# Kernel tuning notes

Measured on AMD Instinct MI355X. Metric: run time of the kernel, lower is better.

The kernel has to match this reference:

```python
import jax, jax.numpy as jnp
import numpy as np

B, S, I, H = 64, 1024, 1024, 1024


def setup_inputs() -> dict:
    key = jax.random.key(0)
    ks = jax.random.split(key, 14)
    bound = (1.0 / H) ** 0.5
    u = lambda k, shape: jax.random.uniform(k, shape, jnp.float32, -bound, bound)
    return {
        "inputs": jax.random.normal(ks[0], (B, S, I), jnp.float32),
        "hidden_states": jax.random.normal(ks[1], (1, B, H), jnp.float32),
        "w_ir": u(ks[2], (H, I)), "w_iz": u(ks[3], (H, I)), "w_in": u(ks[4], (H, I)),
        "b_ir": u(ks[5], (H,)), "b_iz": u(ks[6], (H,)), "b_in": u(ks[7], (H,)),
        "w_hr": u(ks[8], (H, H)), "w_hz": u(ks[9], (H, H)), "w_hn": u(ks[10], (H, H)),
        "b_hr": u(ks[11], (H,)), "b_hz": u(ks[12], (H,)), "b_hn": u(ks[13], (H,)),
    }


def reference(inputs, hidden_states, w_ir, w_iz, w_in, b_ir, b_iz, b_in,
              w_hr, w_hz, w_hn, b_hr, b_hz, b_hn):
    # Precompute input projections for all timesteps (batched GEMMs), [B,S,H]
    x_ir = jnp.einsum('bsi,hi->bsh', inputs, w_ir) + b_ir
    x_iz = jnp.einsum('bsi,hi->bsh', inputs, w_iz) + b_iz
    x_in = jnp.einsum('bsi,hi->bsh', inputs, w_in) + b_in

    def step(h, xs):
        xr, xz, xn = xs  # each [B,H]
        r = jax.nn.sigmoid(xr + h @ w_hr.T + b_hr)
        z = jax.nn.sigmoid(xz + h @ w_hz.T + b_hz)
        n = jnp.tanh(xn + r * (h @ w_hn.T + b_hn))
        h_new = (1.0 - z) * n + z * h
        return h_new, h_new

    h0 = hidden_states[0]  # [B,H]
    # scan over time: xs leading axis S
    xs = (jnp.swapaxes(x_ir, 0, 1), jnp.swapaxes(x_iz, 0, 1), jnp.swapaxes(x_in, 0, 1))
    h_final, outs = jax.lax.scan(step, h0, xs)
    outputs = jnp.swapaxes(outs, 0, 1)  # [B,S,H]
    return outputs, h_final[None]
```

## Files before the change

### kernel.cpp

```cpp
#include <hip/hip_runtime.h>
#include <hip/hip_bf16.h>

typedef __attribute__((ext_vector_type(8))) short bf16x8;
typedef __attribute__((ext_vector_type(4))) float f32x4;
typedef unsigned short u16;
typedef unsigned int u32;

static constexpr int B_ = 64, S_ = 1024, I_ = 1024, H_ = 1024;

__device__ __forceinline__ u16 f2b(float f) {
  union { float f; unsigned u; } v; v.f = f;
  unsigned r = v.u + 0x7FFF + ((v.u >> 16) & 1);
  return (u16)(r >> 16);
}
__device__ __forceinline__ float b2f(u16 u) {
  union { unsigned u; float f; } v; v.u = ((unsigned)u) << 16;
  return v.f;
}

__device__ __forceinline__ void st_coh_u16(void* p, unsigned v) {
  asm volatile("global_store_short %0, %1, off sc0 sc1" :: "v"(p), "v"(v) : "memory");
}
__device__ __forceinline__ void st_coh_u32(void* p, unsigned v) {
  asm volatile("global_store_dword %0, %1, off sc0 sc1" :: "v"(p), "v"(v) : "memory");
}
__device__ __forceinline__ unsigned ld_coh_u32_wait(const void* p) {
  unsigned r;
  asm volatile("global_load_dword %0, %1, off sc0 sc1\n\ts_waitcnt vmcnt(0)"
               : "=v"(r) : "v"(p) : "memory");
  return r;
}
__device__ __forceinline__ uint4 ld_coh_b128(const void* p) {
  uint4 r;
  asm volatile("global_load_dwordx4 %0, %1, off sc0 sc1" : "=v"(r) : "v"(p) : "memory");
  return r;
}

__global__ void cvt_f32_bf16(const float* __restrict__ src, u16* __restrict__ dst, int n4) {
  int i = blockIdx.x * blockDim.x + threadIdx.x;
  int stride = gridDim.x * blockDim.x;
  for (; i < n4; i += stride) {
    float4 f = ((const float4*)src)[i];
    ushort4 o;
    o.x = f2b(f.x); o.y = f2b(f.y); o.z = f2b(f.z); o.w = f2b(f.w);
    ((ushort4*)dst)[i] = o;
  }
}

__global__ __launch_bounds__(256) void xproj_gemm(
    const u16* __restrict__ A, const u16* __restrict__ W,
    const float* __restrict__ b_ir, const float* __restrict__ b_iz, const float* __restrict__ b_in,
    u16* __restrict__ X) {
  __shared__ u16 smem[16384];
  u16* As = smem;
  u16* Bs = smem + 8192;
  int bid = blockIdx.x;
  int mt = bid / 24; int rr = bid % 24; int g = rr >> 3; int nt = rr & 7;
  int tid = threadIdx.x, lane = tid & 63, wid = tid >> 6;
  int wr = wid >> 1, wc = wid & 1;
  const u16* A0 = A + (size_t)mt * 128 * 1024;
  const u16* W0 = W + (size_t)g * 1024 * 1024 + (size_t)nt * 128 * 1024;
  f32x4 acc[4][4] = {};
  for (int k0 = 0; k0 < 1024; k0 += 64) {
    __syncthreads();
#pragma unroll
    for (int j = 0; j < 4; ++j) {
      int c = wid * 4 + j;
      int row = c * 8 + (lane >> 3);
      int ke = (lane & 7) * 8;
      __builtin_amdgcn_global_load_lds(
          (const __attribute__((address_space(1))) void*)(A0 + row * 1024 + k0 + ke),
          (__attribute__((address_space(3))) void*)(As + c * 512), 16, 0, 0);
      __builtin_amdgcn_global_load_lds(
          (const __attribute__((address_space(1))) void*)(W0 + row * 1024 + k0 + ke),
          (__attribute__((address_space(3))) void*)(Bs + c * 512), 16, 0, 0);
    }
    asm volatile("s_waitcnt vmcnt(0)" ::: "memory");
    __syncthreads();
#pragma unroll
    for (int kk = 0; kk < 64; kk += 32) {
      bf16x8 a[4], b[4];
      int rbase = lane & 15;
      int koff = kk + ((lane >> 4) << 3);
#pragma unroll
      for (int mi = 0; mi < 4; ++mi)
        a[mi] = *(const bf16x8*)(As + (wr * 64 + mi * 16 + rbase) * 64 + koff);
#pragma unroll
      for (int ni = 0; ni < 4; ++ni)
        b[ni] = *(const bf16x8*)(Bs + (wc * 64 + ni * 16 + rbase) * 64 + koff);
#pragma unroll
      for (int mi = 0; mi < 4; ++mi)
#pragma unroll
        for (int ni = 0; ni < 4; ++ni)
          acc[mi][ni] = __builtin_amdgcn_mfma_f32_16x16x32_bf16(a[mi], b[ni], acc[mi][ni], 0, 0, 0);
    }
  }
  __syncthreads();
  const float* bp = (g == 0) ? b_ir : (g == 1) ? b_iz : b_in;
  float bias[4];
#pragma unroll
  for (int ni = 0; ni < 4; ++ni)
    bias[ni] = bp[nt * 128 + wc * 64 + ni * 16 + (lane & 15)];
#pragma unroll
  for (int mi = 0; mi < 4; ++mi)
#pragma unroll
    for (int ni = 0; ni < 4; ++ni) {
      int ml = wr * 64 + mi * 16 + ((lane >> 4) << 2);
      int nl = wc * 64 + ni * 16 + (lane & 15);
#pragma unroll
      for (int i = 0; i < 4; ++i)
        smem[(ml + i) * 128 + nl] = f2b(acc[mi][ni][i] + bias[ni]);
    }
  __syncthreads();
#pragma unroll
  for (int j = 0; j < 8; ++j) {
    int c = tid + j * 256;
    int rowl = c >> 4;
    int n0 = (c & 15) * 8;
    int m = mt * 128 + rowl;
    int b = m >> 10, s = m & 1023;
    bf16x8 v = *(const bf16x8*)(smem + rowl * 128 + n0);
    *(bf16x8*)(X + ((size_t)((s * 64 + b) * 3 + g)) * 1024 + nt * 128 + n0) = v;
  }
}

__global__ __launch_bounds__(256) void gru_scan(
    const u16* __restrict__ xbuf, const float* __restrict__ h0p,
    const float* __restrict__ w_hr, const float* __restrict__ w_hz, const float* __restrict__ w_hn,
    const float* __restrict__ b_hr, const float* __restrict__ b_hz, const float* __restrict__ b_hn,
    u16* __restrict__ hbf, float* __restrict__ out, u32* __restrict__ flags) {
  extern __shared__ u16 smem[];
  u16* Wl = smem;
  u16* Hl = smem + 49152;
  float* ex = (float*)(smem + 65536);
  int tid = threadIdx.x, lane = tid & 63, wid = tid >> 6;
  int wg = blockIdx.x, mq = wg & 3, cb = wg >> 2;
  u32* gflags = flags + mq * 64;

  for (int idx = tid; idx < 3 * 2048; idx += 256) {
    int g = idx >> 11; int rem = idx & 2047; int row = rem >> 7; int ch = rem & 127;
    const float* wsrc = (g == 0) ? w_hr : (g == 1) ? w_hz : w_hn;
    const float* src = wsrc + (size_t)(cb * 16 + row) * 1024 + ch * 8;
    float4 f0 = *(const float4*)src;
    float4 f1 = *(const float4*)(src + 4);
    bf16x8 v;
    v[0] = (short)f2b(f0.x); v[1] = (short)f2b(f0.y); v[2] = (short)f2b(f0.z); v[3] = (short)f2b(f0.w);
    v[4] = (short)f2b(f1.x); v[5] = (short)f2b(f1.y); v[6] = (short)f2b(f1.z); v[7] = (short)f2b(f1.w);
    int kbyte = (ch * 16) ^ ((row & 7) << 4);
    *(bf16x8*)((char*)(Wl + g * 16384) + row * 2048 + kbyte) = v;
  }

  int b_l = tid >> 4, c_l = tid & 15;
  int bg = mq * 16 + b_l, cg = cb * 16 + c_l;
  float h = h0p[bg * 1024 + cg];
  float bhr = b_hr[cg], bhz = b_hz[cg], bhn = b_hn[cg];
  st_coh_u16(hbf + bg * 1024 + cg, f2b(h));
  __syncthreads();
  if (tid == 0) st_coh_u32(gflags + cb, 1u);

  bf16x8 wfrag[32];
  {
    const char* wbase = (const char*)(Wl + (wid < 3 ? wid : 0) * 16384);
    int row = lane & 15;
    int klane = (lane >> 4) << 4;
    int sw = (row & 7) << 4;
#pragma unroll
    for (int ks = 0; ks < 32; ++ks)
      wfrag[ks] = *(const bf16x8*)(wbase + row * 2048 + (((ks << 6) + klane) ^ sw));
  }

  const size_t outb = (size_t)bg * S_ * H_;
  for (int t = 0; t < S_; ++t) {
    const u16* rdbuf = hbf + (size_t)(t & 1) * 65536;
    u16* wrbuf = hbf + (size_t)((t + 1) & 1) * 65536;

    const u16* xp = xbuf + (size_t)(t * 64 + bg) * 3072 + cg;
    u16 xr_u = xp[0], xz_u = xp[1024], xn_u = xp[2048];

    {
      unsigned tgt = (unsigned)(t + 1);
      const u32* fp = gflags + lane;
      unsigned v = ld_coh_u32_wait(fp);
      while (!__all((int)(v >= tgt))) {
        __builtin_amdgcn_s_sleep(1);
        v = ld_coh_u32_wait(fp);
      }
    }

    uint4 tmp[8];
#pragma unroll
    for (int j = 0; j < 8; ++j) {
      int ch2 = tid + j * 256;
      int row = ch2 >> 7, kc = ch2 & 127;
      tmp[j] = ld_coh_b128(rdbuf + (mq * 16 + row) * 1024 + kc * 8);
    }
    asm volatile("s_waitcnt vmcnt(0)" ::: "memory");
    __builtin_amdgcn_sched_barrier(0);
#pragma unroll
    for (int j = 0; j < 8; ++j) {
      int ch2 = tid + j * 256;
      int row = ch2 >> 7, kc = ch2 & 127;
      int kbyte = (kc * 16) ^ ((row & 7) << 4);
      *(uint4*)((char*)Hl + row * 2048 + kbyte) = tmp[j];
    }
    __syncthreads();

    f32x4 acc0 = {}, acc1 = {}, acc2 = {}, acc3 = {};
    if (wid < 3) {
      const char* hbase = (const char*)Hl;
      int row = lane & 15;
      int klane = (lane >> 4) << 4;
      int sw = (row & 7) << 4;
#pragma unroll
      for (int ks = 0; ks < 32; ks += 4) {
#pragma unroll
        for (int q = 0; q < 4; ++q) {
          int off = row * 2048 + ((((ks + q) << 6) + klane) ^ sw);
          bf16x8 av = *(const bf16x8*)(hbase + off);
          if (q == 0) acc0 = __builtin_amdgcn_mfma_f32_16x16x32_bf16(av, wfrag[ks + q], acc0, 0, 0, 0);
          else if (q == 1) acc1 = __builtin_amdgcn_mfma_f32_16x16x32_bf16(av, wfrag[ks + q], acc1, 0, 0, 0);
          else if (q == 2) acc2 = __builtin_amdgcn_mfma_f32_16x16x32_bf16(av, wfrag[ks + q], acc2, 0, 0, 0);
          else acc3 = __builtin_amdgcn_mfma_f32_16x16x32_bf16(av, wfrag[ks + q], acc3, 0, 0, 0);
        }
      }
      f32x4 acc = (acc0 + acc1) + (acc2 + acc3);
      int col = lane & 15, r0 = (lane >> 4) << 2;
#pragma unroll
      for (int i = 0; i < 4; ++i)
        ex[wid * 256 + (r0 + i) * 16 + col] = acc[i];
    }
    __syncthreads();

    float hr = ex[b_l * 16 + c_l] + bhr;
    float hz = ex[256 + b_l * 16 + c_l] + bhz;
    float hn = ex[512 + b_l * 16 + c_l] + bhn;
    float xr = b2f(xr_u), xz = b2f(xz_u), xn = b2f(xn_u);
    float r = 1.f / (1.f + __expf(-(xr + hr)));
    float z = 1.f / (1.f + __expf(-(xz + hz)));
    float nn = 1.f - 2.f / (__expf(2.f * (xn + r * hn)) + 1.f);
    h = (1.f - z) * nn + z * h;
    st_coh_u16(wrbuf + bg * 1024 + cg, f2b(h));
    __syncthreads();
    if (tid == 0) st_coh_u32(gflags + cb, (unsigned)(t + 2));
    out[outb + (size_t)t * H_ + cg] = h;
  }
  out[(size_t)B_ * S_ * H_ + bg * 1024 + cg] = h;
}

extern "C" void kernel_launch(void* const* d_in, const int* in_sizes, int n_in,
                              void* d_out, int out_size, void* d_ws, size_t ws_size,
                              hipStream_t stream) {
  const float* inputs = (const float*)d_in[0];
  const float* h0p    = (const float*)d_in[1];
  const float* w_ir   = (const float*)d_in[2];
  const float* w_iz   = (const float*)d_in[3];
  const float* w_in   = (const float*)d_in[4];
  const float* b_ir   = (const float*)d_in[5];
  const float* b_iz   = (const float*)d_in[6];
  const float* b_in   = (const float*)d_in[7];
  const float* w_hr   = (const float*)d_in[8];
  const float* w_hz   = (const float*)d_in[9];
  const float* w_hn   = (const float*)d_in[10];
  const float* b_hr   = (const float*)d_in[11];
  const float* b_hz   = (const float*)d_in[12];
  const float* b_hn   = (const float*)d_in[13];
  float* out = (float*)d_out;

  size_t xbytes  = (size_t)S_ * B_ * 3 * H_ * 2;
  size_t wibytes = (size_t)3 * H_ * I_ * 2;
  size_t hbytes  = (size_t)2 * B_ * H_ * 2;
  size_t flagbytes = 1024;
  if (ws_size < xbytes + wibytes + hbytes + flagbytes) return;

  u16* xbuf = (u16*)d_ws;
  u16* wibf = (u16*)((char*)d_ws + xbytes);
  u16* hbf  = (u16*)((char*)d_ws + xbytes + wibytes);
  u32* flags = (u32*)((char*)d_ws + xbytes + wibytes + hbytes);
  u16* Abf  = (u16*)d_out;

  (void)hipMemsetAsync(flags, 0, flagbytes, stream);

  cvt_f32_bf16<<<2048, 256, 0, stream>>>(inputs, Abf, B_ * S_ * I_ / 4);
  cvt_f32_bf16<<<256, 256, 0, stream>>>(w_ir, wibf,               H_ * I_ / 4);
  cvt_f32_bf16<<<256, 256, 0, stream>>>(w_iz, wibf + H_ * I_,     H_ * I_ / 4);
  cvt_f32_bf16<<<256, 256, 0, stream>>>(w_in, wibf + 2 * H_ * I_, H_ * I_ / 4);

  xproj_gemm<<<12288, 256, 0, stream>>>(Abf, wibf, b_ir, b_iz, b_in, xbuf);

  (void)hipFuncSetAttribute((const void*)gru_scan, hipFuncAttributeMaxDynamicSharedMemorySize, 135168);
  gru_scan<<<dim3(256), dim3(256), 134144, stream>>>(
      xbuf, h0p, w_hr, w_hz, w_hn, b_hr, b_hz, b_hn, hbf, out, flags);
}
```

Measured before the change: 4.592 ms.

## Replace per-step flag barrier with timestep-tagged hidden-state words polled directly

Each hidden-state element is now stored as a 32-bit word holding its bf16 value plus the timestep tag in the upper half. Consumers poll the data itself until every tag matches, instead of waiting on a per-block flag that was written after a block-wide syncthreads. This removes the extra syncthreads, the separate flag store, and the flag-then-data round trip on each step. A per-wave consumption flag guards against the double buffer being overwritten too early. In exchange the hidden-state traffic doubles, and the whole 16-row read is retried on every failed poll.

```diff
diff --git a/kernel.cpp b/kernel.cpp
--- a/kernel.cpp
+++ b/kernel.cpp
@@ -18,17 +18,8 @@
   return v.f;
 }
 
-__device__ __forceinline__ void st_coh_u16(void* p, unsigned v) {
-  asm volatile("global_store_short %0, %1, off sc0 sc1" :: "v"(p), "v"(v) : "memory");
-}
 __device__ __forceinline__ void st_coh_u32(void* p, unsigned v) {
   asm volatile("global_store_dword %0, %1, off sc0 sc1" :: "v"(p), "v"(v) : "memory");
-}
-__device__ __forceinline__ unsigned ld_coh_u32_wait(const void* p) {
-  unsigned r;
-  asm volatile("global_load_dword %0, %1, off sc0 sc1\n\ts_waitcnt vmcnt(0)"
-               : "=v"(r) : "v"(p) : "memory");
-  return r;
 }
 __device__ __forceinline__ uint4 ld_coh_b128(const void* p) {
   uint4 r;
@@ -128,14 +119,13 @@
     const u16* __restrict__ xbuf, const float* __restrict__ h0p,
     const float* __restrict__ w_hr, const float* __restrict__ w_hz, const float* __restrict__ w_hn,
     const float* __restrict__ b_hr, const float* __restrict__ b_hz, const float* __restrict__ b_hn,
-    u16* __restrict__ hbf, float* __restrict__ out, u32* __restrict__ flags) {
+    u32* __restrict__ hbuf, float* __restrict__ out, u32* __restrict__ flags) {
   extern __shared__ u16 smem[];
   u16* Wl = smem;
   u16* Hl = smem + 49152;
   float* ex = (float*)(smem + 65536);
   int tid = threadIdx.x, lane = tid & 63, wid = tid >> 6;
   int wg = blockIdx.x, mq = wg & 3, cb = wg >> 2;
-  u32* gflags = flags + mq * 64;
 
   for (int idx = tid; idx < 3 * 2048; idx += 256) {
     int g = idx >> 11; int rem = idx & 2047; int row = rem >> 7; int ch = rem & 127;
@@ -154,9 +144,8 @@
   int bg = mq * 16 + b_l, cg = cb * 16 + c_l;
   float h = h0p[bg * 1024 + cg];
   float bhr = b_hr[cg], bhz = b_hz[cg], bhn = b_hn[cg];
-  st_coh_u16(hbf + bg * 1024 + cg, f2b(h));
+  st_coh_u32(hbuf + bg * 1024 + cg, (unsigned)f2b(h));
   __syncthreads();
-  if (tid == 0) st_coh_u32(gflags + cb, 1u);
 
   bf16x8 wfrag[32];
   {
@@ -169,39 +158,50 @@
       wfrag[ks] = *(const bf16x8*)(wbase + row * 2048 + (((ks << 6) + klane) ^ sw));
   }
 
+  u32* cfl_self = flags + mq * 256 + wid * 64 + cb;
+  const u32* cfl_poll = flags + mq * 256 + wid * 64 + lane;
   const size_t outb = (size_t)bg * S_ * H_;
+
   for (int t = 0; t < S_; ++t) {
-    const u16* rdbuf = hbf + (size_t)(t & 1) * 65536;
-    u16* wrbuf = hbf + (size_t)((t + 1) & 1) * 65536;
+    const u32* rbase = hbuf + (size_t)(t & 1) * 65536 + (size_t)(mq * 16 + wid * 4) * 1024;
+    u32* wrw = hbuf + (size_t)((t + 1) & 1) * 65536 + bg * 1024 + cg;
 
     const u16* xp = xbuf + (size_t)(t * 64 + bg) * 3072 + cg;
     u16 xr_u = xp[0], xz_u = xp[1024], xn_u = xp[2048];
 
-    {
-      unsigned tgt = (unsigned)(t + 1);
-      const u32* fp = gflags + lane;
-      unsigned v = ld_coh_u32_wait(fp);
-      while (!__all((int)(v >= tgt))) {
-        __builtin_amdgcn_s_sleep(1);
-        v = ld_coh_u32_wait(fp);
+    uint4 tmp[16];
+    unsigned et = (unsigned)t;
+    for (;;) {
+#pragma unroll
+      for (int j = 0; j < 16; ++j) {
+        int cid = j * 64 + lane;
+        int rl = cid >> 8, c4 = cid & 255;
+        tmp[j] = ld_coh_b128(rbase + rl * 1024 + c4 * 4);
       }
-    }
-
-    uint4 tmp[8];
-#pragma unroll
-    for (int j = 0; j < 8; ++j) {
-      int ch2 = tid + j * 256;
-      int row = ch2 >> 7, kc = ch2 & 127;
-      tmp[j] = ld_coh_b128(rdbuf + (mq * 16 + row) * 1024 + kc * 8);
-    }
-    asm volatile("s_waitcnt vmcnt(0)" ::: "memory");
-    __builtin_amdgcn_sched_barrier(0);
-#pragma unroll
-    for (int j = 0; j < 8; ++j) {
-      int ch2 = tid + j * 256;
-      int row = ch2 >> 7, kc = ch2 & 127;
-      int kbyte = (kc * 16) ^ ((row & 7) << 4);
-      *(uint4*)((char*)Hl + row * 2048 + kbyte) = tmp[j];
+      unsigned cf;
+      asm volatile("global_load_dword %0, %1, off sc0 sc1" : "=v"(cf) : "v"(cfl_poll) : "memory");
+      asm volatile("s_waitcnt vmcnt(0)" ::: "memory");
+      __builtin_amdgcn_sched_barrier(0);
+      bool ok = (cf >= et);
+#pragma unroll
+      for (int j = 0; j < 16; ++j)
+        ok = ok & ((tmp[j].x >> 16) == et) & ((tmp[j].y >> 16) == et)
+                & ((tmp[j].z >> 16) == et) & ((tmp[j].w >> 16) == et);
+      if (__all((int)ok)) break;
+      __builtin_amdgcn_s_sleep(1);
+    }
+    if (lane == 0) st_coh_u32(cfl_self, (unsigned)(t + 1));
+
+#pragma unroll
+    for (int j = 0; j < 16; ++j) {
+      int cid = j * 64 + lane;
+      int rl = cid >> 8, c4 = cid & 255;
+      int row = wid * 4 + rl;
+      uint2 pk;
+      pk.x = (tmp[j].x & 0xffffu) | (tmp[j].y << 16);
+      pk.y = (tmp[j].z & 0xffffu) | (tmp[j].w << 16);
+      int kbyte = (c4 * 8) ^ ((row & 7) << 4);
+      *(uint2*)((char*)Hl + row * 2048 + kbyte) = pk;
     }
     __syncthreads();
 
@@ -239,9 +239,7 @@
     float z = 1.f / (1.f + __expf(-(xz + hz)));
     float nn = 1.f - 2.f / (__expf(2.f * (xn + r * hn)) + 1.f);
     h = (1.f - z) * nn + z * h;
-    st_coh_u16(wrbuf + bg * 1024 + cg, f2b(h));
-    __syncthreads();
-    if (tid == 0) st_coh_u32(gflags + cb, (unsigned)(t + 2));
+    st_coh_u32(wrw, ((unsigned)(t + 1) << 16) | (unsigned)f2b(h));
     out[outb + (size_t)t * H_ + cg] = h;
   }
   out[(size_t)B_ * S_ * H_ + bg * 1024 + cg] = h;
@@ -268,16 +266,17 @@
 
   size_t xbytes  = (size_t)S_ * B_ * 3 * H_ * 2;
   size_t wibytes = (size_t)3 * H_ * I_ * 2;
-  size_t hbytes  = (size_t)2 * B_ * H_ * 2;
-  size_t flagbytes = 1024;
+  size_t hbytes  = (size_t)2 * B_ * H_ * 4;
+  size_t flagbytes = 4096;
   if (ws_size < xbytes + wibytes + hbytes + flagbytes) return;
 
   u16* xbuf = (u16*)d_ws;
   u16* wibf = (u16*)((char*)d_ws + xbytes);
-  u16* hbf  = (u16*)((char*)d_ws + xbytes + wibytes);
+  u32* hbuf = (u32*)((char*)d_ws + xbytes + wibytes);
   u32* flags = (u32*)((char*)d_ws + xbytes + wibytes + hbytes);
   u16* Abf  = (u16*)d_out;
 
+  (void)hipMemsetAsync(hbuf, 0xFF, hbytes, stream);
   (void)hipMemsetAsync(flags, 0, flagbytes, stream);
 
   cvt_f32_bf16<<<2048, 256, 0, stream>>>(inputs, Abf, B_ * S_ * I_ / 4);
@@ -289,5 +288,5 @@
 
   (void)hipFuncSetAttribute((const void*)gru_scan, hipFuncAttributeMaxDynamicSharedMemorySize, 135168);
   gru_scan<<<dim3(256), dim3(256), 134144, stream>>>(
-      xbuf, h0p, w_hr, w_hz, w_hn, b_hr, b_hz, b_hn, hbf, out, flags);
-}
+      xbuf, h0p, w_hr, w_hz, w_hn, b_hr, b_hz, b_hn, hbuf, out, flags);
+}
```

New measurement: 6.520 ms. +42.0%, slower.

## Fuse input projection GEMM into persistent GRU scan kernel

Applied to the files above, without the earlier changes.

Removes the separate xproj_gemm kernel and the large bf16 X buffer. Each scan workgroup now keeps its slice of the input weights in registers and computes the input projection for its batch rows each timestep. It prefetches the next timestep's bf16 inputs into a double-buffered LDS tile and overlaps this work with the flag wait for the hidden state. This trades a bulk-parallel GEMM plus its memory round trip for extra MFMA work and input loads inside the serial scan loop, and it raises register pressure with a second 32-entry weight-fragment array.

```diff
diff --git a/kernel.cpp b/kernel.cpp
--- a/kernel.cpp
+++ b/kernel.cpp
@@ -12,10 +12,6 @@
   union { float f; unsigned u; } v; v.f = f;
   unsigned r = v.u + 0x7FFF + ((v.u >> 16) & 1);
   return (u16)(r >> 16);
-}
-__device__ __forceinline__ float b2f(u16 u) {
-  union { unsigned u; float f; } v; v.u = ((unsigned)u) << 16;
-  return v.f;
 }
 
 __device__ __forceinline__ void st_coh_u16(void* p, unsigned v) {
@@ -47,135 +43,117 @@
   }
 }
 
-__global__ __launch_bounds__(256) void xproj_gemm(
-    const u16* __restrict__ A, const u16* __restrict__ W,
+__global__ __launch_bounds__(256) void gru_scan(
+    const u16* __restrict__ Abf, const u16* __restrict__ wib, const float* __restrict__ h0p,
+    const float* __restrict__ w_hr, const float* __restrict__ w_hz, const float* __restrict__ w_hn,
     const float* __restrict__ b_ir, const float* __restrict__ b_iz, const float* __restrict__ b_in,
-    u16* __restrict__ X) {
-  __shared__ u16 smem[16384];
-  u16* As = smem;
-  u16* Bs = smem + 8192;
-  int bid = blockIdx.x;
-  int mt = bid / 24; int rr = bid % 24; int g = rr >> 3; int nt = rr & 7;
-  int tid = threadIdx.x, lane = tid & 63, wid = tid >> 6;
-  int wr = wid >> 1, wc = wid & 1;
-  const u16* A0 = A + (size_t)mt * 128 * 1024;
-  const u16* W0 = W + (size_t)g * 1024 * 1024 + (size_t)nt * 128 * 1024;
-  f32x4 acc[4][4] = {};
-  for (int k0 = 0; k0 < 1024; k0 += 64) {
-    __syncthreads();
-#pragma unroll
-    for (int j = 0; j < 4; ++j) {
-      int c = wid * 4 + j;
-      int row = c * 8 + (lane >> 3);
-      int ke = (lane & 7) * 8;
-      __builtin_amdgcn_global_load_lds(
-          (const __attribute__((address_space(1))) void*)(A0 + row * 1024 + k0 + ke),
-          (__attribute__((address_space(3))) void*)(As + c * 512), 16, 0, 0);
-      __builtin_amdgcn_global_load_lds(
-          (const __attribute__((address_space(1))) void*)(W0 + row * 1024 + k0 + ke),
-          (__attribute__((address_space(3))) void*)(Bs + c * 512), 16, 0, 0);
-    }
-    asm volatile("s_waitcnt vmcnt(0)" ::: "memory");
-    __syncthreads();
-#pragma unroll
-    for (int kk = 0; kk < 64; kk += 32) {
-      bf16x8 a[4], b[4];
-      int rbase = lane & 15;
-      int koff = kk + ((lane >> 4) << 3);
-#pragma unroll
-      for (int mi = 0; mi < 4; ++mi)
-        a[mi] = *(const bf16x8*)(As + (wr * 64 + mi * 16 + rbase) * 64 + koff);
-#pragma unroll
-      for (int ni = 0; ni < 4; ++ni)
-        b[ni] = *(const bf16x8*)(Bs + (wc * 64 + ni * 16 + rbase) * 64 + koff);
-#pragma unroll
-      for (int mi = 0; mi < 4; ++mi)
-#pragma unroll
-        for (int ni = 0; ni < 4; ++ni)
-          acc[mi][ni] = __builtin_amdgcn_mfma_f32_16x16x32_bf16(a[mi], b[ni], acc[mi][ni], 0, 0, 0);
-    }
-  }
-  __syncthreads();
-  const float* bp = (g == 0) ? b_ir : (g == 1) ? b_iz : b_in;
-  float bias[4];
-#pragma unroll
-  for (int ni = 0; ni < 4; ++ni)
-    bias[ni] = bp[nt * 128 + wc * 64 + ni * 16 + (lane & 15)];
-#pragma unroll
-  for (int mi = 0; mi < 4; ++mi)
-#pragma unroll
-    for (int ni = 0; ni < 4; ++ni) {
-      int ml = wr * 64 + mi * 16 + ((lane >> 4) << 2);
-      int nl = wc * 64 + ni * 16 + (lane & 15);
-#pragma unroll
-      for (int i = 0; i < 4; ++i)
-        smem[(ml + i) * 128 + nl] = f2b(acc[mi][ni][i] + bias[ni]);
-    }
-  __syncthreads();
-#pragma unroll
-  for (int j = 0; j < 8; ++j) {
-    int c = tid + j * 256;
-    int rowl = c >> 4;
-    int n0 = (c & 15) * 8;
-    int m = mt * 128 + rowl;
-    int b = m >> 10, s = m & 1023;
-    bf16x8 v = *(const bf16x8*)(smem + rowl * 128 + n0);
-    *(bf16x8*)(X + ((size_t)((s * 64 + b) * 3 + g)) * 1024 + nt * 128 + n0) = v;
-  }
-}
-
-__global__ __launch_bounds__(256) void gru_scan(
-    const u16* __restrict__ xbuf, const float* __restrict__ h0p,
-    const float* __restrict__ w_hr, const float* __restrict__ w_hz, const float* __restrict__ w_hn,
     const float* __restrict__ b_hr, const float* __restrict__ b_hz, const float* __restrict__ b_hn,
     u16* __restrict__ hbf, float* __restrict__ out, u32* __restrict__ flags) {
-  extern __shared__ u16 smem[];
-  u16* Wl = smem;
-  u16* Hl = smem + 49152;
-  float* ex = (float*)(smem + 65536);
+  extern __shared__ char lds[];
+  char* Hl = lds + 65536;
+  float* ex = (float*)(lds + 98304);
   int tid = threadIdx.x, lane = tid & 63, wid = tid >> 6;
   int wg = blockIdx.x, mq = wg & 3, cb = wg >> 2;
   u32* gflags = flags + mq * 64;
+  int b_l = tid >> 4, c_l = tid & 15;
+  int bg = mq * 16 + b_l, cg = cb * 16 + c_l;
+  int row = lane & 15, klane = (lane >> 4) << 4, sw = (row & 7) << 4;
 
   for (int idx = tid; idx < 3 * 2048; idx += 256) {
-    int g = idx >> 11; int rem = idx & 2047; int row = rem >> 7; int ch = rem & 127;
+    int g = idx >> 11, rem = idx & 2047, r2 = rem >> 7, ch = rem & 127;
+    bf16x8 v = *(const bf16x8*)(wib + (size_t)g * 1048576 + (size_t)(cb * 16 + r2) * 1024 + ch * 8);
+    int kbyte = (ch * 16) ^ ((r2 & 7) << 4);
+    *(bf16x8*)(lds + g * 32768 + r2 * 2048 + kbyte) = v;
+  }
+  __syncthreads();
+  bf16x8 wfragI[32];
+  {
+    const char* wb = lds + (wid < 3 ? wid : 0) * 32768;
+#pragma unroll
+    for (int ks = 0; ks < 32; ++ks)
+      wfragI[ks] = *(const bf16x8*)(wb + row * 2048 + (((ks << 6) + klane) ^ sw));
+  }
+  __syncthreads();
+  for (int idx = tid; idx < 3 * 2048; idx += 256) {
+    int g = idx >> 11, rem = idx & 2047, r2 = rem >> 7, ch = rem & 127;
     const float* wsrc = (g == 0) ? w_hr : (g == 1) ? w_hz : w_hn;
-    const float* src = wsrc + (size_t)(cb * 16 + row) * 1024 + ch * 8;
+    const float* src = wsrc + (size_t)(cb * 16 + r2) * 1024 + ch * 8;
     float4 f0 = *(const float4*)src;
     float4 f1 = *(const float4*)(src + 4);
     bf16x8 v;
     v[0] = (short)f2b(f0.x); v[1] = (short)f2b(f0.y); v[2] = (short)f2b(f0.z); v[3] = (short)f2b(f0.w);
     v[4] = (short)f2b(f1.x); v[5] = (short)f2b(f1.y); v[6] = (short)f2b(f1.z); v[7] = (short)f2b(f1.w);
-    int kbyte = (ch * 16) ^ ((row & 7) << 4);
-    *(bf16x8*)((char*)(Wl + g * 16384) + row * 2048 + kbyte) = v;
-  }
-
-  int b_l = tid >> 4, c_l = tid & 15;
-  int bg = mq * 16 + b_l, cg = cb * 16 + c_l;
+    int kbyte = (ch * 16) ^ ((r2 & 7) << 4);
+    *(bf16x8*)(lds + g * 32768 + r2 * 2048 + kbyte) = v;
+  }
+  __syncthreads();
+  bf16x8 wfrag[32];
+  {
+    const char* wb = lds + (wid < 3 ? wid : 0) * 32768;
+#pragma unroll
+    for (int ks = 0; ks < 32; ++ks)
+      wfrag[ks] = *(const bf16x8*)(wb + row * 2048 + (((ks << 6) + klane) ^ sw));
+  }
+  __syncthreads();
+
   float h = h0p[bg * 1024 + cg];
   float bhr = b_hr[cg], bhz = b_hz[cg], bhn = b_hn[cg];
-  st_coh_u16(hbf + bg * 1024 + cg, f2b(h));
-  __syncthreads();
-  if (tid == 0) st_coh_u32(gflags + cb, 1u);
-
-  bf16x8 wfrag[32];
+  float bir = b_ir[cg], biz = b_iz[cg], bin = b_in[cg];
+
   {
-    const char* wbase = (const char*)(Wl + (wid < 3 ? wid : 0) * 16384);
-    int row = lane & 15;
-    int klane = (lane >> 4) << 4;
-    int sw = (row & 7) << 4;
-#pragma unroll
-    for (int ks = 0; ks < 32; ++ks)
-      wfrag[ks] = *(const bf16x8*)(wbase + row * 2048 + (((ks << 6) + klane) ^ sw));
+    uint4 tx[8];
+#pragma unroll
+    for (int j = 0; j < 8; ++j) {
+      int ch2 = tid + j * 256;
+      int r2 = ch2 >> 7, kc = ch2 & 127;
+      tx[j] = *(const uint4*)(Abf + ((size_t)((mq * 16 + r2) * 1024 + 0)) * 1024 + kc * 8);
+    }
+    st_coh_u16(hbf + bg * 1024 + cg, f2b(h));
+    asm volatile("s_waitcnt vmcnt(0)" ::: "memory");
+    __builtin_amdgcn_sched_barrier(0);
+#pragma unroll
+    for (int j = 0; j < 8; ++j) {
+      int ch2 = tid + j * 256;
+      int r2 = ch2 >> 7, kc = ch2 & 127;
+      int kbyte = (kc * 16) ^ ((r2 & 7) << 4);
+      *(uint4*)(lds + r2 * 2048 + kbyte) = tx[j];
+    }
+    __syncthreads();
+    if (tid == 0) st_coh_u32(gflags + cb, 1u);
   }
 
   const size_t outb = (size_t)bg * S_ * H_;
   for (int t = 0; t < S_; ++t) {
     const u16* rdbuf = hbf + (size_t)(t & 1) * 65536;
     u16* wrbuf = hbf + (size_t)((t + 1) & 1) * 65536;
-
-    const u16* xp = xbuf + (size_t)(t * 64 + bg) * 3072 + cg;
-    u16 xr_u = xp[0], xz_u = xp[1024], xn_u = xp[2048];
+    const char* Xcur = lds + (size_t)(t & 1) * 32768;
+    char* Xnxt = lds + (size_t)((t + 1) & 1) * 32768;
+
+    int tn = (t + 1 < S_) ? t + 1 : t;
+    uint4 tx[8];
+#pragma unroll
+    for (int j = 0; j < 8; ++j) {
+      int ch2 = tid + j * 256;
+      int r2 = ch2 >> 7, kc = ch2 & 127;
+      tx[j] = *(const uint4*)(Abf + ((size_t)((mq * 16 + r2) * 1024 + tn)) * 1024 + kc * 8);
+    }
+
+    f32x4 ax0 = {}, ax1 = {}, ax2 = {}, ax3 = {};
+    f32x4 ah0 = {}, ah1 = {}, ah2 = {}, ah3 = {};
+    if (wid < 3) {
+#pragma unroll
+      for (int ks = 0; ks < 32; ks += 4) {
+#pragma unroll
+        for (int q = 0; q < 4; ++q) {
+          int off = row * 2048 + ((((ks + q) << 6) + klane) ^ sw);
+          bf16x8 av = *(const bf16x8*)(Xcur + off);
+          if (q == 0) ax0 = __builtin_amdgcn_mfma_f32_16x16x32_bf16(av, wfragI[ks + q], ax0, 0, 0, 0);
+          else if (q == 1) ax1 = __builtin_amdgcn_mfma_f32_16x16x32_bf16(av, wfragI[ks + q], ax1, 0, 0, 0);
+          else if (q == 2) ax2 = __builtin_amdgcn_mfma_f32_16x16x32_bf16(av, wfragI[ks + q], ax2, 0, 0, 0);
+          else ax3 = __builtin_amdgcn_mfma_f32_16x16x32_bf16(av, wfragI[ks + q], ax3, 0, 0, 0);
+        }
+      }
+    }
 
     {
       unsigned tgt = (unsigned)(t + 1);
@@ -191,52 +169,58 @@
 #pragma unroll
     for (int j = 0; j < 8; ++j) {
       int ch2 = tid + j * 256;
-      int row = ch2 >> 7, kc = ch2 & 127;
-      tmp[j] = ld_coh_b128(rdbuf + (mq * 16 + row) * 1024 + kc * 8);
+      int r2 = ch2 >> 7, kc = ch2 & 127;
+      tmp[j] = ld_coh_b128(rdbuf + (mq * 16 + r2) * 1024 + kc * 8);
     }
     asm volatile("s_waitcnt vmcnt(0)" ::: "memory");
     __builtin_amdgcn_sched_barrier(0);
 #pragma unroll
     for (int j = 0; j < 8; ++j) {
       int ch2 = tid + j * 256;
-      int row = ch2 >> 7, kc = ch2 & 127;
-      int kbyte = (kc * 16) ^ ((row & 7) << 4);
-      *(uint4*)((char*)Hl + row * 2048 + kbyte) = tmp[j];
-    }
-    __syncthreads();
-
-    f32x4 acc0 = {}, acc1 = {}, acc2 = {}, acc3 = {};
+      int r2 = ch2 >> 7, kc = ch2 & 127;
+      int kbyte = (kc * 16) ^ ((r2 & 7) << 4);
+      *(uint4*)(Hl + r2 * 2048 + kbyte) = tmp[j];
+      *(uint4*)(Xnxt + r2 * 2048 + kbyte) = tx[j];
+    }
+    __syncthreads();
+
     if (wid < 3) {
-      const char* hbase = (const char*)Hl;
-      int row = lane & 15;
-      int klane = (lane >> 4) << 4;
-      int sw = (row & 7) << 4;
 #pragma unroll
       for (int ks = 0; ks < 32; ks += 4) {
 #pragma unroll
         for (int q = 0; q < 4; ++q) {
           int off = row * 2048 + ((((ks + q) << 6) + klane) ^ sw);
-          bf16x8 av = *(const bf16x8*)(hbase + off);
-          if (q == 0) acc0 = __builtin_amdgcn_mfma_f32_16x16x32_bf16(av, wfrag[ks + q], acc0, 0, 0, 0);
-          else if (q == 1) acc1 = __builtin_amdgcn_mfma_f32_16x16x32_bf16(av, wfrag[ks + q], acc1, 0, 0, 0);
-          else if (q == 2) acc2 = __builtin_amdgcn_mfma_f32_16x16x32_bf16(av, wfrag[ks + q], acc2, 0, 0, 0);
-          else acc3 = __builtin_amdgcn_mfma_f32_16x16x32_bf16(av, wfrag[ks + q], acc3, 0, 0, 0);
+          bf16x8 av = *(const bf16x8*)(Hl + off);
+          if (q == 0) ah0 = __builtin_amdgcn_mfma_f32_16x16x32_bf16(av, wfrag[ks + q], ah0, 0, 0, 0);
+          else if (q == 1) ah1 = __builtin_amdgcn_mfma_f32_16x16x32_bf16(av, wfrag[ks + q], ah1, 0, 0, 0);
+          else if (q == 2) ah2 = __builtin_amdgcn_mfma_f32_16x16x32_bf16(av, wfrag[ks + q], ah2, 0, 0, 0);
+          else ah3 = __builtin_amdgcn_mfma_f32_16x16x32_bf16(av, wfrag[ks + q], ah3, 0, 0, 0);
         }
       }
-      f32x4 acc = (acc0 + acc1) + (acc2 + acc3);
+      f32x4 ax = (ax0 + ax1) + (ax2 + ax3);
+      f32x4 ah = (ah0 + ah1) + (ah2 + ah3);
       int col = lane & 15, r0 = (lane >> 4) << 2;
-#pragma unroll
-      for (int i = 0; i < 4; ++i)
-        ex[wid * 256 + (r0 + i) * 16 + col] = acc[i];
-    }
-    __syncthreads();
-
-    float hr = ex[b_l * 16 + c_l] + bhr;
-    float hz = ex[256 + b_l * 16 + c_l] + bhz;
-    float hn = ex[512 + b_l * 16 + c_l] + bhn;
-    float xr = b2f(xr_u), xz = b2f(xz_u), xn = b2f(xn_u);
-    float r = 1.f / (1.f + __expf(-(xr + hr)));
-    float z = 1.f / (1.f + __expf(-(xz + hz)));
+      if (wid < 2) {
+        f32x4 a = ax + ah;
+#pragma unroll
+        for (int i = 0; i < 4; ++i)
+          ex[wid * 256 + (r0 + i) * 16 + col] = a[i];
+      } else {
+#pragma unroll
+        for (int i = 0; i < 4; ++i) {
+          ex[512 + (r0 + i) * 16 + col] = ax[i];
+          ex[768 + (r0 + i) * 16 + col] = ah[i];
+        }
+      }
+    }
+    __syncthreads();
+
+    float sr = ex[b_l * 16 + c_l] + bir + bhr;
+    float sz = ex[256 + b_l * 16 + c_l] + biz + bhz;
+    float xn = ex[512 + b_l * 16 + c_l] + bin;
+    float hn = ex[768 + b_l * 16 + c_l] + bhn;
+    float r = 1.f / (1.f + __expf(-sr));
+    float z = 1.f / (1.f + __expf(-sz));
     float nn = 1.f - 2.f / (__expf(2.f * (xn + r * hn)) + 1.f);
     h = (1.f - z) * nn + z * h;
     st_coh_u16(wrbuf + bg * 1024 + cg, f2b(h));
@@ -266,17 +250,16 @@
   const float* b_hn   = (const float*)d_in[13];
   float* out = (float*)d_out;
 
-  size_t xbytes  = (size_t)S_ * B_ * 3 * H_ * 2;
+  size_t abytes  = (size_t)B_ * S_ * I_ * 2;
   size_t wibytes = (size_t)3 * H_ * I_ * 2;
   size_t hbytes  = (size_t)2 * B_ * H_ * 2;
   size_t flagbytes = 1024;
-  if (ws_size < xbytes + wibytes + hbytes + flagbytes) return;
-
-  u16* xbuf = (u16*)d_ws;
-  u16* wibf = (u16*)((char*)d_ws + xbytes);
-  u16* hbf  = (u16*)((char*)d_ws + xbytes + wibytes);
-  u32* flags = (u32*)((char*)d_ws + xbytes + wibytes + hbytes);
-  u16* Abf  = (u16*)d_out;
+  if (ws_size < abytes + wibytes + hbytes + flagbytes) return;
+
+  u16* Abf  = (u16*)d_ws;
+  u16* wibf = (u16*)((char*)d_ws + abytes);
+  u16* hbf  = (u16*)((char*)d_ws + abytes + wibytes);
+  u32* flags = (u32*)((char*)d_ws + abytes + wibytes + hbytes);
 
   (void)hipMemsetAsync(flags, 0, flagbytes, stream);
 
@@ -285,9 +268,8 @@
   cvt_f32_bf16<<<256, 256, 0, stream>>>(w_iz, wibf + H_ * I_,     H_ * I_ / 4);
   cvt_f32_bf16<<<256, 256, 0, stream>>>(w_in, wibf + 2 * H_ * I_, H_ * I_ / 4);
 
-  xproj_gemm<<<12288, 256, 0, stream>>>(Abf, wibf, b_ir, b_iz, b_in, xbuf);
-
-  (void)hipFuncSetAttribute((const void*)gru_scan, hipFuncAttributeMaxDynamicSharedMemorySize, 135168);
-  gru_scan<<<dim3(256), dim3(256), 134144, stream>>>(
-      xbuf, h0p, w_hr, w_hz, w_hn, b_hr, b_hz, b_hn, hbf, out, flags);
-}
+  (void)hipFuncSetAttribute((const void*)gru_scan, hipFuncAttributeMaxDynamicSharedMemorySize, 102400);
+  gru_scan<<<dim3(256), dim3(256), 102400, stream>>>(
+      Abf, wibf, h0p, w_hr, w_hz, w_hn, b_ir, b_iz, b_in, b_hr, b_hz, b_hn,
+      hbf, out, flags);
+}
```

New measurement: 6.643 ms. 1.45x slower.
